# Performance work log

Measured on AMD Instinct MI355X. Metric: run time of the kernel, lower is better.

The kernel has to match this reference:

```python
import math
import jax, jax.numpy as jnp
import numpy as np

N_HEAD = 12
LN_EPS = 1e-5

def _gelu(x):
    # NewGELU: tanh approximation
    c = math.sqrt(2.0 / math.pi)
    return 0.5 * x * (1.0 + jnp.tanh(c * (x + 0.044715 * x ** 3)))

def _ln(x, w, b):
    m = x.mean(-1, keepdims=True)
    v = x.var(-1, keepdims=True)
    return (x - m) / jnp.sqrt(v + LN_EPS) * w + b

def setup_inputs() -> dict:
    key = jax.random.key(0)
    ks = jax.random.split(key, 8)
    L, C, V, BS = 12, 768, 30522, 1024
    B, T = 4, 1024
    std = 0.02
    inp = {
        'idx': jax.random.randint(ks[0], (B, T), 0, V),
        'wte': jax.random.normal(ks[1], (V, C), jnp.float32) * std,
        'wpe': jax.random.normal(ks[2], (BS, C), jnp.float32) * std,
        'ln1_w': jnp.ones((L, C), jnp.float32),
        'ln1_b': jnp.zeros((L, C), jnp.float32),
        'attn_w': jax.random.normal(ks[3], (L, 3 * C, C), jnp.float32) * std,
        'attn_b': jnp.zeros((L, 3 * C), jnp.float32),
        'proj_w': jax.random.normal(ks[4], (L, C, C), jnp.float32) * (std / math.sqrt(2 * L)),
        'proj_b': jnp.zeros((L, C), jnp.float32),
        'ln2_w': jnp.ones((L, C), jnp.float32),
        'ln2_b': jnp.zeros((L, C), jnp.float32),
        'fc_w': jax.random.normal(ks[5], (L, 4 * C, C), jnp.float32) * std,
        'fc_b': jnp.zeros((L, 4 * C), jnp.float32),
        'mproj_w': jax.random.normal(ks[6], (L, C, 4 * C), jnp.float32) * (std / math.sqrt(2 * L)),
        'mproj_b': jnp.zeros((L, C), jnp.float32),
        'lnf_w': jnp.ones((C,), jnp.float32),
        'lnf_b': jnp.zeros((C,), jnp.float32),
        'lm_head_w': jax.random.normal(ks[7], (V, C), jnp.float32) * std,
    }
    return inp

def reference(idx, wte, wpe, ln1_w, ln1_b, attn_w, attn_b, proj_w, proj_b,
              ln2_w, ln2_b, fc_w, fc_b, mproj_w, mproj_b, lnf_w, lnf_b, lm_head_w):
    B, T = idx.shape
    C = wte.shape[1]
    H = N_HEAD
    D = C // H
    scale = 1.0 / math.sqrt(D)
    x = wte[idx] + wpe[:T][None]  # [B,T,C], drop is identity (p=0)

    def block(x, p):
        l1w, l1b, aw, ab, pw, pb, l2w, l2b, fw, fb, mw, mb = p
        h = _ln(x, l1w, l1b)
        qkv = jnp.einsum('btc,ec->bte', h, aw) + ab  # [B,T,3C]
        q, k, v = jnp.split(qkv, 3, axis=-1)
        q = q.reshape(B, T, H, D)
        k = k.reshape(B, T, H, D)
        v = v.reshape(B, T, H, D)
        att = jnp.einsum('bthd,bshd->bhts', q, k) * scale  # [B,H,T,T]
        att = jax.nn.softmax(att, axis=-1)  # mask=None: full attention
        y = jnp.einsum('bhts,bshd->bthd', att, v).reshape(B, T, C)
        x = x + jnp.einsum('btc,oc->bto', y, pw) + pb
        h = _gelu(jnp.einsum('btc,fc->btf', _ln(x, l2w, l2b), fw) + fb)
        x = x + jnp.einsum('btf,cf->btc', h, mw) + mb
        return x, None

    x, _ = jax.lax.scan(block, x, (ln1_w, ln1_b, attn_w, attn_b, proj_w, proj_b,
                                   ln2_w, ln2_b, fc_w, fc_b, mproj_w, mproj_b))
    x = _ln(x, lnf_w, lnf_b)
    logits = jnp.einsum('btc,vc->btv', x, lm_head_w)  # [B,T,V]
    return logits
```

## Files before the change

kernel.cpp:

```cpp
#include <hip/hip_runtime.h>
#include <hip/hip_bf16.h>
#include <math.h>

typedef __attribute__((ext_vector_type(8))) short short8;
typedef __attribute__((ext_vector_type(4))) float f32x4;

typedef unsigned short u16;

__device__ __forceinline__ u16 f2bf(float f) {
    union { float f; unsigned int u; } v; v.f = f;
    unsigned int u = v.u;
    unsigned int r = (u + 0x7fffu + ((u >> 16) & 1u)) >> 16;
    return (u16)r;
}
__device__ __forceinline__ float bf2f(u16 u) {
    union { unsigned int u; float f; } v; v.u = ((unsigned int)u) << 16;
    return v.f;
}

__device__ __forceinline__ void gload16(const void* g, void* l) {
    __builtin_amdgcn_global_load_lds(
        (const __attribute__((address_space(1))) void*)g,
        (__attribute__((address_space(3))) void*)l, 16, 0, 0);
}

__global__ __launch_bounds__(256) void castw_kernel(const float* __restrict__ src,
                                                    u16* __restrict__ dst,
                                                    long n, long npad) {
    long i = ((long)blockIdx.x * 256 + threadIdx.x) * 4;
    const long stride = (long)gridDim.x * 1024;
    for (; i < npad; i += stride) {
        ushort4 o;
        if (i < n) {
            float4 v = *reinterpret_cast<const float4*>(src + i);
            o.x = f2bf(v.x); o.y = f2bf(v.y); o.z = f2bf(v.z); o.w = f2bf(v.w);
        } else {
            o = make_ushort4(0, 0, 0, 0);
        }
        *reinterpret_cast<ushort4*>(dst + i) = o;
    }
}

__global__ __launch_bounds__(256) void embed_kernel(const int* __restrict__ idx,
                                                    const float* __restrict__ wte,
                                                    const float* __restrict__ wpe,
                                                    float* __restrict__ x) {
    const int row = blockIdx.x;
    const int tid = threadIdx.x;
    const int t = row & 1023;
    const int tok = idx[row];
    const float* we = wte + (size_t)tok * 768;
    const float* pe = wpe + (size_t)t * 768;
    float* xr = x + (size_t)row * 768;
    xr[tid]       = we[tid]       + pe[tid];
    xr[tid + 256] = we[tid + 256] + pe[tid + 256];
    xr[tid + 512] = we[tid + 512] + pe[tid + 512];
}

__global__ __launch_bounds__(256) void ln_kernel(const float* __restrict__ x,
                                                 const float* __restrict__ w,
                                                 const float* __restrict__ b,
                                                 u16* __restrict__ out) {
    const int row = blockIdx.x;
    const int tid = threadIdx.x;
    const float* xr = x + (size_t)row * 768;
    float v0 = xr[tid], v1 = xr[tid + 256], v2 = xr[tid + 512];
    float s = v0 + v1 + v2;
    float q = v0 * v0 + v1 * v1 + v2 * v2;
    #pragma unroll
    for (int off = 32; off >= 1; off >>= 1) {
        s += __shfl_xor(s, off);
        q += __shfl_xor(q, off);
    }
    __shared__ float rs[4], rq[4];
    const int wid = tid >> 6, lane = tid & 63;
    if (lane == 0) { rs[wid] = s; rq[wid] = q; }
    __syncthreads();
    s = rs[0] + rs[1] + rs[2] + rs[3];
    q = rq[0] + rq[1] + rq[2] + rq[3];
    const float mean = s * (1.f / 768.f);
    const float var = q * (1.f / 768.f) - mean * mean;
    const float rstd = rsqrtf(var + 1e-5f);
    u16* orow = out + (size_t)row * 768;
    orow[tid]       = f2bf((v0 - mean) * rstd * w[tid]       + b[tid]);
    orow[tid + 256] = f2bf((v1 - mean) * rstd * w[tid + 256] + b[tid + 256]);
    orow[tid + 512] = f2bf((v2 - mean) * rstd * w[tid + 512] + b[tid + 512]);
}

template<int EPI>
__global__ __launch_bounds__(512) void gemm_big(
        const u16* __restrict__ A, int lda,
        const u16* __restrict__ B, int ldb,
        const float* __restrict__ bias,
        void* __restrict__ Cout, int ldc,
        int N, int K, int nmt) {
    __shared__ __align__(16) u16 lds[2][384 * 32];
    const int tid = threadIdx.x;
    const int lane = tid & 63, wid = tid >> 6;
    const int nwg = gridDim.x;
    const int o = blockIdx.x;
    const int wg = (o & 7) * (nwg >> 3) + (o >> 3);
    const int m0 = (wg % nmt) * 256, n0 = (wg / nmt) * 128;

    const int wm = (wid >> 1) * 64, wn = (wid & 1) * 64;
    const int l16 = lane & 15;
    const int qid = lane >> 4;
    const int xq8 = ((qid ^ (l16 & 3)) * 8);

    const int ar = tid >> 2, aq = (tid & 3) ^ (ar & 3);
    const size_t a_src0 = (size_t)(m0 + ar) * lda + aq * 8;
    const size_t a_src1 = (size_t)(m0 + ar + 128) * lda + aq * 8;
    const int br = tid >> 2, bq = (tid & 3) ^ (br & 3);
    const size_t b_src = (size_t)(n0 + br) * ldb + bq * 8;

    f32x4 acc[4][4];
    #pragma unroll
    for (int i = 0; i < 4; i++)
        #pragma unroll
        for (int j = 0; j < 4; j++)
            acc[i][j] = (f32x4){0.f, 0.f, 0.f, 0.f};

    const int nk = K >> 5;
    gload16(A + a_src0, lds[0] + tid * 8);
    gload16(A + a_src1, lds[0] + tid * 8 + 4096);
    gload16(B + b_src,  lds[0] + tid * 8 + 8192);

    for (int t = 0; t < nk; ++t) {
        if (t + 1 < nk) {
            u16* buf = lds[(t + 1) & 1];
            const int k0 = (t + 1) << 5;
            gload16(A + a_src0 + k0, buf + tid * 8);
            gload16(A + a_src1 + k0, buf + tid * 8 + 4096);
            gload16(B + b_src + k0,  buf + tid * 8 + 8192);
            asm volatile("s_waitcnt vmcnt(3)" ::: "memory");
        } else {
            asm volatile("s_waitcnt vmcnt(0)" ::: "memory");
        }
        __builtin_amdgcn_s_barrier();
        asm volatile("" ::: "memory");
        const u16* As = lds[t & 1];
        const u16* Bs = lds[t & 1] + 8192;
        short8 af[4], bf[4];
        #pragma unroll
        for (int i = 0; i < 4; i++) {
            af[i] = *reinterpret_cast<const short8*>(&As[(wm + i * 16 + l16) * 32 + xq8]);
            bf[i] = *reinterpret_cast<const short8*>(&Bs[(wn + i * 16 + l16) * 32 + xq8]);
        }
        #pragma unroll
        for (int mi = 0; mi < 4; mi++)
            #pragma unroll
            for (int ni = 0; ni < 4; ni++)
                acc[mi][ni] = __builtin_amdgcn_mfma_f32_16x16x32_bf16(af[mi], bf[ni], acc[mi][ni], 0, 0, 0);
        asm volatile("" ::: "memory");
        __builtin_amdgcn_s_barrier();
    }

    if (EPI == 3) {
        float* ct = reinterpret_cast<float*>(&lds[0][0]) + wid * 1088;
        const int rw = (lane >> 4) * 4;
        const int rr = lane >> 2;
        const int rc = (lane & 3) * 16;
        #pragma unroll
        for (int mi = 0; mi < 4; mi++) {
            asm volatile("" ::: "memory");
            #pragma unroll
            for (int ni = 0; ni < 4; ni++)
                #pragma unroll
                for (int j = 0; j < 4; j++)
                    ct[(rw + j) * 68 + ni * 16 + l16] = acc[mi][ni][j];
            asm volatile("" ::: "memory");
            const int m = m0 + wm + mi * 16 + rr;
            const int nb = n0 + wn + rc;
            float* crow = (float*)Cout + (size_t)m * ldc + nb;
            #pragma unroll
            for (int q = 0; q < 4; q++) {
                const f32x4 v = *reinterpret_cast<const f32x4*>(&ct[rr * 68 + rc + q * 4]);
                if (nb + q * 4 + 3 < N) {
                    *reinterpret_cast<f32x4*>(crow + q * 4) = v;
                } else {
                    #pragma unroll
                    for (int e = 0; e < 4; e++)
                        if (nb + q * 4 + e < N) crow[q * 4 + e] = v[e];
                }
            }
            asm volatile("" ::: "memory");
            __builtin_amdgcn_s_barrier();
        }
    } else {
        const int cb = n0 + wn + l16;
        const int rb = m0 + wm + (lane >> 4) * 4;
        #pragma unroll
        for (int ni = 0; ni < 4; ni++) {
            const int n = cb + ni * 16;
            const float bv = bias[n];
            #pragma unroll
            for (int mi = 0; mi < 4; mi++) {
                #pragma unroll
                for (int j = 0; j < 4; j++) {
                    const int m = rb + mi * 16 + j;
                    float v = acc[mi][ni][j] + bv;
                    if (EPI == 0) {
                        ((u16*)Cout)[(size_t)m * ldc + n] = f2bf(v);
                    } else {
                        const float t = tanhf(0.7978845608028654f * (v + 0.044715f * v * v * v));
                        ((u16*)Cout)[(size_t)m * ldc + n] = f2bf(0.5f * v * (1.f + t));
                    }
                }
            }
        }
    }
}

template<int EPI>
__global__ __launch_bounds__(256) void gemm_bb(
        const u16* __restrict__ A, int lda,
        const u16* __restrict__ B, int ldb,
        const float* __restrict__ bias,
        void* __restrict__ Cout, int ldc,
        int N, int K, int nmt,
        float* __restrict__ resid) {
    __shared__ __align__(16) u16 lds[2][2][128 * 32];
    const int tid = threadIdx.x;
    const int lane = tid & 63, wid = tid >> 6;
    const int nwg = gridDim.x;
    const int o = blockIdx.x;
    const int wg = (o & 7) * (nwg >> 3) + (o >> 3);
    const int m0 = (wg % nmt) * 128, n0 = (wg / nmt) * 128;

    const int wm = (wid >> 1) * 64, wn = (wid & 1) * 64;
    const int l16 = lane & 15;
    const int qid = lane >> 4;
    const int xq8 = ((qid ^ (l16 & 3)) * 8);

    const int r0 = tid >> 2, q0 = (tid & 3) ^ (r0 & 3);
    const size_t a_src0 = (size_t)(m0 + r0) * lda + q0 * 8;
    const size_t a_src1 = (size_t)(m0 + r0 + 64) * lda + q0 * 8;
    const size_t b_src0 = (size_t)(n0 + r0) * ldb + q0 * 8;
    const size_t b_src1 = (size_t)(n0 + r0 + 64) * ldb + q0 * 8;

    f32x4 acc[4][4];
    #pragma unroll
    for (int i = 0; i < 4; i++)
        #pragma unroll
        for (int j = 0; j < 4; j++)
            acc[i][j] = (f32x4){0.f, 0.f, 0.f, 0.f};

    const int nk = K >> 5;
    gload16(A + a_src0, lds[0][0] + tid * 8);
    gload16(A + a_src1, lds[0][0] + tid * 8 + 2048);
    gload16(B + b_src0, lds[0][1] + tid * 8);
    gload16(B + b_src1, lds[0][1] + tid * 8 + 2048);

    for (int t = 0; t < nk; ++t) {
        if (t + 1 < nk) {
            u16* Ap = lds[(t + 1) & 1][0];
            u16* Bp = lds[(t + 1) & 1][1];
            const int k0 = (t + 1) << 5;
            gload16(A + a_src0 + k0, Ap + tid * 8);
            gload16(A + a_src1 + k0, Ap + tid * 8 + 2048);
            gload16(B + b_src0 + k0, Bp + tid * 8);
            gload16(B + b_src1 + k0, Bp + tid * 8 + 2048);
            asm volatile("s_waitcnt vmcnt(4)" ::: "memory");
        } else {
            asm volatile("s_waitcnt vmcnt(0)" ::: "memory");
        }
        __builtin_amdgcn_s_barrier();
        asm volatile("" ::: "memory");
        const u16* As = lds[t & 1][0];
        const u16* Bs = lds[t & 1][1];
        short8 af[4], bf[4];
        #pragma unroll
        for (int i = 0; i < 4; i++) {
            af[i] = *reinterpret_cast<const short8*>(&As[(wm + i * 16 + l16) * 32 + xq8]);
            bf[i] = *reinterpret_cast<const short8*>(&Bs[(wn + i * 16 + l16) * 32 + xq8]);
        }
        #pragma unroll
        for (int mi = 0; mi < 4; mi++)
            #pragma unroll
            for (int ni = 0; ni < 4; ni++)
                acc[mi][ni] = __builtin_amdgcn_mfma_f32_16x16x32_bf16(af[mi], bf[ni], acc[mi][ni], 0, 0, 0);
        asm volatile("" ::: "memory");
        __builtin_amdgcn_s_barrier();
    }

    const int cb = n0 + wn + l16;
    const int rb = m0 + wm + (lane >> 4) * 4;
    #pragma unroll
    for (int ni = 0; ni < 4; ni++) {
        const int n = cb + ni * 16;
        const float bv = bias[n];
        #pragma unroll
        for (int mi = 0; mi < 4; mi++) {
            #pragma unroll
            for (int j = 0; j < 4; j++) {
                const int m = rb + mi * 16 + j;
                float v = acc[mi][ni][j] + bv;
                if (EPI == 1) {
                    resid[(size_t)m * ldc + n] += v;
                } else if (EPI == 0) {
                    ((u16*)Cout)[(size_t)m * ldc + n] = f2bf(v);
                } else {
                    const float t = tanhf(0.7978845608028654f * (v + 0.044715f * v * v * v));
                    ((u16*)Cout)[(size_t)m * ldc + n] = f2bf(0.5f * v * (1.f + t));
                }
            }
        }
    }
}

template<int EPI>
__global__ __launch_bounds__(256, 2) void gemm_bt(
        const u16* __restrict__ A, int lda,
        const float* __restrict__ B, int ldb,
        const float* __restrict__ bias,
        void* __restrict__ Cout, int ldc,
        int M, int N, int K,
        float* __restrict__ resid) {
    __shared__ __align__(16) u16 As[128][40];
    __shared__ __align__(16) u16 Bs[128][40];
    const int tid = threadIdx.x;
    const int lane = tid & 63, wid = tid >> 6;
    const int m0 = blockIdx.y * 128, n0 = blockIdx.x * 128;
    const int wm = (wid >> 1) * 64, wn = (wid & 1) * 64;
    const int l16 = lane & 15, lk = (lane >> 4) * 8;

    f32x4 acc[4][4];
    #pragma unroll
    for (int i = 0; i < 4; i++)
        #pragma unroll
        for (int j = 0; j < 4; j++)
            acc[i][j] = (f32x4){0.f, 0.f, 0.f, 0.f};

    for (int k0 = 0; k0 < K; k0 += 32) {
        #pragma unroll
        for (int p = 0; p < 2; p++) {
            const int e = p * 256 + tid;
            const int r = e >> 2, c = e & 3;
            uint4 v = *reinterpret_cast<const uint4*>(A + (size_t)(m0 + r) * lda + k0 + c * 8);
            *reinterpret_cast<uint4*>(&As[r][c * 8]) = v;
        }
        #pragma unroll
        for (int p = 0; p < 4; p++) {
            const int e = p * 256 + tid;
            const int r = e >> 3, c = e & 7;
            float4 v = make_float4(0.f, 0.f, 0.f, 0.f);
            if (n0 + r < N)
                v = *reinterpret_cast<const float4*>(B + (size_t)(n0 + r) * ldb + k0 + c * 4);
            ushort4 hv;
            hv.x = f2bf(v.x); hv.y = f2bf(v.y); hv.z = f2bf(v.z); hv.w = f2bf(v.w);
            *reinterpret_cast<ushort4*>(&Bs[r][c * 4]) = hv;
        }
        __syncthreads();
        short8 af[4], bfr[4];
        #pragma unroll
        for (int i = 0; i < 4; i++) {
            af[i]  = *reinterpret_cast<const short8*>(&As[wm + i * 16 + l16][lk]);
            bfr[i] = *reinterpret_cast<const short8*>(&Bs[wn + i * 16 + l16][lk]);
        }
        #pragma unroll
        for (int mi = 0; mi < 4; mi++)
            #pragma unroll
            for (int ni = 0; ni < 4; ni++)
                acc[mi][ni] = __builtin_amdgcn_mfma_f32_16x16x32_bf16(af[mi], bfr[ni], acc[mi][ni], 0, 0, 0);
        __syncthreads();
    }

    const int cb = n0 + wn + l16;
    const int rb = m0 + wm + (lane >> 4) * 4;
    #pragma unroll
    for (int ni = 0; ni < 4; ni++) {
        const int n = cb + ni * 16;
        if (n >= N) continue;
        float bv = 0.f;
        if (EPI != 3) bv = bias[n];
        #pragma unroll
        for (int mi = 0; mi < 4; mi++) {
            #pragma unroll
            for (int j = 0; j < 4; j++) {
                const int m = rb + mi * 16 + j;
                float v = acc[mi][ni][j] + bv;
                if (EPI == 0) {
                    ((u16*)Cout)[(size_t)m * ldc + n] = f2bf(v);
                } else if (EPI == 1) {
                    resid[(size_t)m * ldc + n] += v;
                } else if (EPI == 2) {
                    const float t = tanhf(0.7978845608028654f * (v + 0.044715f * v * v * v));
                    ((u16*)Cout)[(size_t)m * ldc + n] = f2bf(0.5f * v * (1.f + t));
                } else {
                    ((float*)Cout)[(size_t)m * ldc + n] = v;
                }
            }
        }
    }
}

__global__ __launch_bounds__(256, 2) void attn_mfma_kernel(const u16* __restrict__ qkv,
                                                           u16* __restrict__ y) {
    __shared__ __align__(16) u16 Qs[64][72];
    __shared__ __align__(16) u16 Ks[64][72];
    __shared__ __align__(16) u16 Vt[64][72];
    __shared__ __align__(16) u16 Ps[4][16][72];

    const int tid = threadIdx.x;
    const int lane = tid & 63, wid = tid >> 6;
    const int l16 = lane & 15, lk = (lane >> 4) * 8;
    const int qt = blockIdx.x, h = blockIdx.y, b = blockIdx.z;

    const size_t base = (size_t)b * 1024 * 2304;
    const u16* qp = qkv + base + (size_t)(qt * 64) * 2304 + h * 64;
    const u16* kp = qkv + base + 768  + h * 64;
    const u16* vp = qkv + base + 1536 + h * 64;

    #pragma unroll
    for (int p = 0; p < 2; p++) {
        const int e = p * 256 + tid;
        const int rr = e >> 3, c8 = e & 7;
        *reinterpret_cast<uint4*>(&Qs[rr][c8 * 8]) =
            *reinterpret_cast<const uint4*>(qp + (size_t)rr * 2304 + c8 * 8);
    }
    __syncthreads();

    short8 qf[2];
    #pragma unroll
    for (int kk = 0; kk < 2; kk++)
        qf[kk] = *reinterpret_cast<const short8*>(&Qs[wid * 16 + l16][kk * 32 + lk]);

    f32x4 o_acc[4];
    #pragma unroll
    for (int i = 0; i < 4; i++) o_acc[i] = (f32x4){0.f, 0.f, 0.f, 0.f};
    float l_part[4] = {0.f, 0.f, 0.f, 0.f};

    for (int s0 = 0; s0 < 1024; s0 += 64) {
        __syncthreads();
        #pragma unroll
        for (int p = 0; p < 2; p++) {
            const int e = p * 256 + tid;
            const int rr = e >> 3, c8 = e & 7;
            *reinterpret_cast<uint4*>(&Ks[rr][c8 * 8]) =
                *reinterpret_cast<const uint4*>(kp + (size_t)(s0 + rr) * 2304 + c8 * 8);
        }
        #pragma unroll
        for (int p = 0; p < 2; p++) {
            const int e = p * 256 + tid;
            const int s2 = e >> 4;
            const int dq = e & 15;
            const int s = s2 * 2;
            ushort4 v0 = *reinterpret_cast<const ushort4*>(vp + (size_t)(s0 + s) * 2304 + dq * 4);
            ushort4 v1 = *reinterpret_cast<const ushort4*>(vp + (size_t)(s0 + s + 1) * 2304 + dq * 4);
            *reinterpret_cast<ushort2*>(&Vt[dq * 4 + 0][s]) = make_ushort2(v0.x, v1.x);
            *reinterpret_cast<ushort2*>(&Vt[dq * 4 + 1][s]) = make_ushort2(v0.y, v1.y);
            *reinterpret_cast<ushort2*>(&Vt[dq * 4 + 2][s]) = make_ushort2(v0.z, v1.z);
            *reinterpret_cast<ushort2*>(&Vt[dq * 4 + 3][s]) = make_ushort2(v0.w, v1.w);
        }
        __syncthreads();

        f32x4 sa[4];
        #pragma unroll
        for (int i = 0; i < 4; i++) sa[i] = (f32x4){0.f, 0.f, 0.f, 0.f};
        #pragma unroll
        for (int nj = 0; nj < 4; nj++) {
            #pragma unroll
            for (int kk = 0; kk < 2; kk++) {
                short8 kf = *reinterpret_cast<const short8*>(&Ks[nj * 16 + l16][kk * 32 + lk]);
                sa[nj] = __builtin_amdgcn_mfma_f32_16x16x32_bf16(qf[kk], kf, sa[nj], 0, 0, 0);
            }
        }

        #pragma unroll
        for (int nj = 0; nj < 4; nj++) {
            #pragma unroll
            for (int r = 0; r < 4; r++) {
                const float pv = __expf(sa[nj][r] * 0.125f);
                l_part[r] += pv;
                Ps[wid][(lane >> 4) * 4 + r][nj * 16 + l16] = f2bf(pv);
            }
        }

        short8 pa[2];
        #pragma unroll
        for (int kk = 0; kk < 2; kk++)
            pa[kk] = *reinterpret_cast<const short8*>(&Ps[wid][l16][kk * 32 + lk]);
        #pragma unroll
        for (int nd = 0; nd < 4; nd++) {
            #pragma unroll
            for (int kk = 0; kk < 2; kk++) {
                short8 vf = *reinterpret_cast<const short8*>(&Vt[nd * 16 + l16][kk * 32 + lk]);
                o_acc[nd] = __builtin_amdgcn_mfma_f32_16x16x32_bf16(pa[kk], vf, o_acc[nd], 0, 0, 0);
            }
        }
    }

    float inv[4];
    #pragma unroll
    for (int r = 0; r < 4; r++) {
        float s = l_part[r];
        #pragma unroll
        for (int off = 8; off >= 1; off >>= 1) s += __shfl_xor(s, off);
        inv[r] = 1.f / s;
    }
    const int rowb = b * 1024 + qt * 64 + wid * 16 + (lane >> 4) * 4;
    #pragma unroll
    for (int nd = 0; nd < 4; nd++) {
        const int col = h * 64 + nd * 16 + l16;
        #pragma unroll
        for (int r = 0; r < 4; r++) {
            y[(size_t)(rowb + r) * 768 + col] = f2bf(o_acc[nd][r] * inv[r]);
        }
    }
}

extern "C" void kernel_launch(void* const* d_in, const int* in_sizes, int n_in,
                              void* d_out, int out_size, void* d_ws, size_t ws_size,
                              hipStream_t stream) {
    (void)in_sizes; (void)n_in; (void)out_size;
    const int*   idx    = (const int*)d_in[0];
    const float* wte    = (const float*)d_in[1];
    const float* wpe    = (const float*)d_in[2];
    const float* ln1w   = (const float*)d_in[3];
    const float* ln1b   = (const float*)d_in[4];
    const float* attnw  = (const float*)d_in[5];
    const float* attnb  = (const float*)d_in[6];
    const float* projw  = (const float*)d_in[7];
    const float* projb  = (const float*)d_in[8];
    const float* ln2w   = (const float*)d_in[9];
    const float* ln2b   = (const float*)d_in[10];
    const float* fcw    = (const float*)d_in[11];
    const float* fcb    = (const float*)d_in[12];
    const float* mprojw = (const float*)d_in[13];
    const float* mprojb = (const float*)d_in[14];
    const float* lnfw   = (const float*)d_in[15];
    const float* lnfb   = (const float*)d_in[16];
    const float* lmw    = (const float*)d_in[17];
    float* out = (float*)d_out;

    char* p = (char*)d_ws;
    size_t used = 0;
    auto take = [&](size_t bytes) { char* q = p + used; used += (bytes + 255) & ~(size_t)255; return q; };
    float* x      = (float*)take((size_t)4096 * 768 * 4);
    u16*   a_bf   = (u16*)take((size_t)4096 * 768 * 2);
    u16*   qkv_bf = (u16*)take((size_t)4096 * 2304 * 2);
    u16*   hid_bf = (u16*)take((size_t)4096 * 3072 * 2);
    u16*   w_lm   = (u16*)take((size_t)30592 * 768 * 2);
    const bool castLm = used <= ws_size;
    u16*   w_attn = (u16*)take((size_t)12 * 2304 * 768 * 2);
    u16*   w_proj = (u16*)take((size_t)12 * 768 * 768 * 2);
    u16*   w_fc   = (u16*)take((size_t)12 * 3072 * 768 * 2);
    u16*   w_mprj = (u16*)take((size_t)12 * 768 * 3072 * 2);
    const bool castAll = used <= ws_size;

    embed_kernel<<<4096, 256, 0, stream>>>(idx, wte, wpe, x);

    if (castLm)
        castw_kernel<<<2048, 256, 0, stream>>>(lmw, w_lm, (long)30522 * 768, (long)30592 * 768);
    if (castAll) {
        castw_kernel<<<2048, 256, 0, stream>>>(attnw,  w_attn, (long)12 * 2304 * 768, (long)12 * 2304 * 768);
        castw_kernel<<<2048, 256, 0, stream>>>(projw,  w_proj, (long)12 * 768 * 768,  (long)12 * 768 * 768);
        castw_kernel<<<2048, 256, 0, stream>>>(fcw,    w_fc,   (long)12 * 3072 * 768, (long)12 * 3072 * 768);
        castw_kernel<<<2048, 256, 0, stream>>>(mprojw, w_mprj, (long)12 * 768 * 3072, (long)12 * 768 * 3072);
    }

    for (int l = 0; l < 12; l++) {
        ln_kernel<<<4096, 256, 0, stream>>>(x, ln1w + l * 768, ln1b + l * 768, a_bf);
        if (castAll) {
            gemm_big<0><<<16 * 18, 512, 0, stream>>>(
                a_bf, 768, w_attn + (size_t)l * 2304 * 768, 768, attnb + l * 2304,
                (void*)qkv_bf, 2304, 2304, 768, 16);
        } else {
            gemm_bt<0><<<dim3(18, 32), 256, 0, stream>>>(
                a_bf, 768, attnw + (size_t)l * 2304 * 768, 768, attnb + l * 2304,
                (void*)qkv_bf, 2304, 4096, 2304, 768, nullptr);
        }
        attn_mfma_kernel<<<dim3(16, 12, 4), 256, 0, stream>>>(qkv_bf, a_bf);
        if (castAll) {
            gemm_bb<1><<<32 * 6, 256, 0, stream>>>(
                a_bf, 768, w_proj + (size_t)l * 768 * 768, 768, projb + l * 768,
                nullptr, 768, 768, 768, 32, x);
        } else {
            gemm_bt<1><<<dim3(6, 32), 256, 0, stream>>>(
                a_bf, 768, projw + (size_t)l * 768 * 768, 768, projb + l * 768,
                nullptr, 768, 4096, 768, 768, x);
        }
        ln_kernel<<<4096, 256, 0, stream>>>(x, ln2w + l * 768, ln2b + l * 768, a_bf);
        if (castAll) {
            gemm_big<2><<<16 * 24, 512, 0, stream>>>(
                a_bf, 768, w_fc + (size_t)l * 3072 * 768, 768, fcb + l * 3072,
                (void*)hid_bf, 3072, 3072, 768, 16);
            gemm_bb<1><<<32 * 6, 256, 0, stream>>>(
                hid_bf, 3072, w_mprj + (size_t)l * 768 * 3072, 3072, mprojb + l * 768,
                nullptr, 768, 768, 3072, 32, x);
        } else {
            gemm_bt<2><<<dim3(24, 32), 256, 0, stream>>>(
                a_bf, 768, fcw + (size_t)l * 3072 * 768, 768, fcb + l * 3072,
                (void*)hid_bf, 3072, 4096, 3072, 768, nullptr);
            gemm_bt<1><<<dim3(6, 32), 256, 0, stream>>>(
                hid_bf, 3072, mprojw + (size_t)l * 768 * 3072, 3072, mprojb + l * 768,
                nullptr, 768, 4096, 768, 3072, x);
        }
    }

    ln_kernel<<<4096, 256, 0, stream>>>(x, lnfw, lnfb, a_bf);
    if (castLm) {
        gemm_big<3><<<16 * 239, 512, 0, stream>>>(
            a_bf, 768, w_lm, 768, nullptr, (void*)out, 30522, 30522, 768, 16);
    } else {
        gemm_bt<3><<<dim3(239, 32), 256, 0, stream>>>(
            a_bf, 768, lmw, 768, nullptr, (void*)out, 30522, 4096, 30522, 768, nullptr);
    }
}
```

Baseline: 3.031 ms.

## Split-K residual GEMMs, pipeline attention K/V loads, warp-per-row LN, reorder LM-head tiles

Replaces the proj and mlp-proj GEMMs with split-K kernels that atomically add partial sums into the fp32 residual, doubling or quadrupling the workgroup count. Adds register-staged double buffering of K/V tiles in the attention kernel so global loads overlap the MFMA work. Rewrites layernorm to one wavefront per row with float4 loads and no shared-memory reduction. Adds an ORDER template so the LM-head GEMM walks N-tiles fastest. Atomics make the residual sum order nondeterministic and add contention on x.

```diff
diff --git a/kernel.cpp b/kernel.cpp
--- a/kernel.cpp
+++ b/kernel.cpp
@@ -61,33 +61,41 @@
                                                  const float* __restrict__ w,
                                                  const float* __restrict__ b,
                                                  u16* __restrict__ out) {
-    const int row = blockIdx.x;
-    const int tid = threadIdx.x;
+    const int wid = threadIdx.x >> 6, lane = threadIdx.x & 63;
+    const int row = blockIdx.x * 4 + wid;
     const float* xr = x + (size_t)row * 768;
-    float v0 = xr[tid], v1 = xr[tid + 256], v2 = xr[tid + 512];
-    float s = v0 + v1 + v2;
-    float q = v0 * v0 + v1 * v1 + v2 * v2;
+    const float4 v0 = *reinterpret_cast<const float4*>(xr + lane * 4);
+    const float4 v1 = *reinterpret_cast<const float4*>(xr + 256 + lane * 4);
+    const float4 v2 = *reinterpret_cast<const float4*>(xr + 512 + lane * 4);
+    float s = v0.x + v0.y + v0.z + v0.w + v1.x + v1.y + v1.z + v1.w
+            + v2.x + v2.y + v2.z + v2.w;
+    float q = v0.x * v0.x + v0.y * v0.y + v0.z * v0.z + v0.w * v0.w
+            + v1.x * v1.x + v1.y * v1.y + v1.z * v1.z + v1.w * v1.w
+            + v2.x * v2.x + v2.y * v2.y + v2.z * v2.z + v2.w * v2.w;
     #pragma unroll
     for (int off = 32; off >= 1; off >>= 1) {
         s += __shfl_xor(s, off);
         q += __shfl_xor(q, off);
     }
-    __shared__ float rs[4], rq[4];
-    const int wid = tid >> 6, lane = tid & 63;
-    if (lane == 0) { rs[wid] = s; rq[wid] = q; }
-    __syncthreads();
-    s = rs[0] + rs[1] + rs[2] + rs[3];
-    q = rq[0] + rq[1] + rq[2] + rq[3];
     const float mean = s * (1.f / 768.f);
     const float var = q * (1.f / 768.f) - mean * mean;
     const float rstd = rsqrtf(var + 1e-5f);
     u16* orow = out + (size_t)row * 768;
-    orow[tid]       = f2bf((v0 - mean) * rstd * w[tid]       + b[tid]);
-    orow[tid + 256] = f2bf((v1 - mean) * rstd * w[tid + 256] + b[tid + 256]);
-    orow[tid + 512] = f2bf((v2 - mean) * rstd * w[tid + 512] + b[tid + 512]);
-}
-
-template<int EPI>
+    #pragma unroll
+    for (int seg = 0; seg < 3; seg++) {
+        const float4 v = seg == 0 ? v0 : (seg == 1 ? v1 : v2);
+        const float4 wv = *reinterpret_cast<const float4*>(w + seg * 256 + lane * 4);
+        const float4 bv = *reinterpret_cast<const float4*>(b + seg * 256 + lane * 4);
+        ushort4 ov;
+        ov.x = f2bf((v.x - mean) * rstd * wv.x + bv.x);
+        ov.y = f2bf((v.y - mean) * rstd * wv.y + bv.y);
+        ov.z = f2bf((v.z - mean) * rstd * wv.z + bv.z);
+        ov.w = f2bf((v.w - mean) * rstd * wv.w + bv.w);
+        *reinterpret_cast<ushort4*>(orow + seg * 256 + lane * 4) = ov;
+    }
+}
+
+template<int EPI, int ORDER>
 __global__ __launch_bounds__(512) void gemm_big(
         const u16* __restrict__ A, int lda,
         const u16* __restrict__ B, int ldb,
@@ -100,7 +108,9 @@
     const int nwg = gridDim.x;
     const int o = blockIdx.x;
     const int wg = (o & 7) * (nwg >> 3) + (o >> 3);
-    const int m0 = (wg % nmt) * 256, n0 = (wg / nmt) * 128;
+    int m0, n0;
+    if (ORDER == 0) { m0 = (wg % nmt) * 256; n0 = (wg / nmt) * 128; }
+    else            { n0 = (wg % nmt) * 128; m0 = (wg / nmt) * 256; }
 
     const int wm = (wid >> 1) * 64, wn = (wid & 1) * 64;
     const int l16 = lane & 15;
@@ -110,8 +120,7 @@
     const int ar = tid >> 2, aq = (tid & 3) ^ (ar & 3);
     const size_t a_src0 = (size_t)(m0 + ar) * lda + aq * 8;
     const size_t a_src1 = (size_t)(m0 + ar + 128) * lda + aq * 8;
-    const int br = tid >> 2, bq = (tid & 3) ^ (br & 3);
-    const size_t b_src = (size_t)(n0 + br) * ldb + bq * 8;
+    const size_t b_src = (size_t)(n0 + ar) * ldb + aq * 8;
 
     f32x4 acc[4][4];
     #pragma unroll
@@ -211,13 +220,11 @@
     }
 }
 
-template<int EPI>
-__global__ __launch_bounds__(256) void gemm_bb(
+__global__ __launch_bounds__(256) void gemm_splitk(
         const u16* __restrict__ A, int lda,
         const u16* __restrict__ B, int ldb,
         const float* __restrict__ bias,
-        void* __restrict__ Cout, int ldc,
-        int N, int K, int nmt,
+        int ldc, int Kp, int nmt, int ntiles,
         float* __restrict__ resid) {
     __shared__ __align__(16) u16 lds[2][2][128 * 32];
     const int tid = threadIdx.x;
@@ -225,7 +232,10 @@
     const int nwg = gridDim.x;
     const int o = blockIdx.x;
     const int wg = (o & 7) * (nwg >> 3) + (o >> 3);
-    const int m0 = (wg % nmt) * 128, n0 = (wg / nmt) * 128;
+    const int tile = wg % ntiles;
+    const int ks = wg / ntiles;
+    const int m0 = (tile % nmt) * 128, n0 = (tile / nmt) * 128;
+    const int koff = ks * Kp;
 
     const int wm = (wid >> 1) * 64, wn = (wid & 1) * 64;
     const int l16 = lane & 15;
@@ -233,10 +243,10 @@
     const int xq8 = ((qid ^ (l16 & 3)) * 8);
 
     const int r0 = tid >> 2, q0 = (tid & 3) ^ (r0 & 3);
-    const size_t a_src0 = (size_t)(m0 + r0) * lda + q0 * 8;
-    const size_t a_src1 = (size_t)(m0 + r0 + 64) * lda + q0 * 8;
-    const size_t b_src0 = (size_t)(n0 + r0) * ldb + q0 * 8;
-    const size_t b_src1 = (size_t)(n0 + r0 + 64) * ldb + q0 * 8;
+    const size_t a_src0 = (size_t)(m0 + r0) * lda + koff + q0 * 8;
+    const size_t a_src1 = (size_t)(m0 + r0 + 64) * lda + koff + q0 * 8;
+    const size_t b_src0 = (size_t)(n0 + r0) * ldb + koff + q0 * 8;
+    const size_t b_src1 = (size_t)(n0 + r0 + 64) * ldb + koff + q0 * 8;
 
     f32x4 acc[4][4];
     #pragma unroll
@@ -245,7 +255,7 @@
         for (int j = 0; j < 4; j++)
             acc[i][j] = (f32x4){0.f, 0.f, 0.f, 0.f};
 
-    const int nk = K >> 5;
+    const int nk = Kp >> 5;
     gload16(A + a_src0, lds[0][0] + tid * 8);
     gload16(A + a_src1, lds[0][0] + tid * 8 + 2048);
     gload16(B + b_src0, lds[0][1] + tid * 8);
@@ -288,21 +298,13 @@
     #pragma unroll
     for (int ni = 0; ni < 4; ni++) {
         const int n = cb + ni * 16;
-        const float bv = bias[n];
+        const float bv = (ks == 0) ? bias[n] : 0.f;
         #pragma unroll
         for (int mi = 0; mi < 4; mi++) {
             #pragma unroll
             for (int j = 0; j < 4; j++) {
                 const int m = rb + mi * 16 + j;
-                float v = acc[mi][ni][j] + bv;
-                if (EPI == 1) {
-                    resid[(size_t)m * ldc + n] += v;
-                } else if (EPI == 0) {
-                    ((u16*)Cout)[(size_t)m * ldc + n] = f2bf(v);
-                } else {
-                    const float t = tanhf(0.7978845608028654f * (v + 0.044715f * v * v * v));
-                    ((u16*)Cout)[(size_t)m * ldc + n] = f2bf(0.5f * v * (1.f + t));
-                }
+                atomicAdd(&resid[(size_t)m * ldc + n], acc[mi][ni][j] + bv);
             }
         }
     }
@@ -397,8 +399,8 @@
 __global__ __launch_bounds__(256, 2) void attn_mfma_kernel(const u16* __restrict__ qkv,
                                                            u16* __restrict__ y) {
     __shared__ __align__(16) u16 Qs[64][72];
-    __shared__ __align__(16) u16 Ks[64][72];
-    __shared__ __align__(16) u16 Vt[64][72];
+    __shared__ __align__(16) u16 Ks[2][64][72];
+    __shared__ __align__(16) u16 Vt[2][64][72];
     __shared__ __align__(16) u16 Ps[4][16][72];
 
     const int tid = threadIdx.x;
@@ -410,6 +412,11 @@
     const u16* qp = qkv + base + (size_t)(qt * 64) * 2304 + h * 64;
     const u16* kp = qkv + base + 768  + h * 64;
     const u16* vp = qkv + base + 1536 + h * 64;
+
+    const int krr0 = tid >> 3, kc8_0 = tid & 7;
+    const int krr1 = (tid + 256) >> 3, kc8_1 = tid & 7;
+    const int vs0 = (tid >> 4) * 2, vdq0 = tid & 15;
+    const int vs1 = ((tid + 256) >> 4) * 2, vdq1 = tid & 15;
 
     #pragma unroll
     for (int p = 0; p < 2; p++) {
@@ -418,6 +425,13 @@
         *reinterpret_cast<uint4*>(&Qs[rr][c8 * 8]) =
             *reinterpret_cast<const uint4*>(qp + (size_t)rr * 2304 + c8 * 8);
     }
+    uint4 kreg0, kreg1; ushort4 vr0a, vr0b, vr1a, vr1b;
+    kreg0 = *reinterpret_cast<const uint4*>(kp + (size_t)krr0 * 2304 + kc8_0 * 8);
+    kreg1 = *reinterpret_cast<const uint4*>(kp + (size_t)krr1 * 2304 + kc8_1 * 8);
+    vr0a = *reinterpret_cast<const ushort4*>(vp + (size_t)vs0 * 2304 + vdq0 * 4);
+    vr0b = *reinterpret_cast<const ushort4*>(vp + (size_t)(vs0 + 1) * 2304 + vdq0 * 4);
+    vr1a = *reinterpret_cast<const ushort4*>(vp + (size_t)vs1 * 2304 + vdq1 * 4);
+    vr1b = *reinterpret_cast<const ushort4*>(vp + (size_t)(vs1 + 1) * 2304 + vdq1 * 4);
     __syncthreads();
 
     short8 qf[2];
@@ -425,34 +439,34 @@
     for (int kk = 0; kk < 2; kk++)
         qf[kk] = *reinterpret_cast<const short8*>(&Qs[wid * 16 + l16][kk * 32 + lk]);
 
+    *reinterpret_cast<uint4*>(&Ks[0][krr0][kc8_0 * 8]) = kreg0;
+    *reinterpret_cast<uint4*>(&Ks[0][krr1][kc8_1 * 8]) = kreg1;
+    *reinterpret_cast<ushort2*>(&Vt[0][vdq0 * 4 + 0][vs0]) = make_ushort2(vr0a.x, vr0b.x);
+    *reinterpret_cast<ushort2*>(&Vt[0][vdq0 * 4 + 1][vs0]) = make_ushort2(vr0a.y, vr0b.y);
+    *reinterpret_cast<ushort2*>(&Vt[0][vdq0 * 4 + 2][vs0]) = make_ushort2(vr0a.z, vr0b.z);
+    *reinterpret_cast<ushort2*>(&Vt[0][vdq0 * 4 + 3][vs0]) = make_ushort2(vr0a.w, vr0b.w);
+    *reinterpret_cast<ushort2*>(&Vt[0][vdq1 * 4 + 0][vs1]) = make_ushort2(vr1a.x, vr1b.x);
+    *reinterpret_cast<ushort2*>(&Vt[0][vdq1 * 4 + 1][vs1]) = make_ushort2(vr1a.y, vr1b.y);
+    *reinterpret_cast<ushort2*>(&Vt[0][vdq1 * 4 + 2][vs1]) = make_ushort2(vr1a.z, vr1b.z);
+    *reinterpret_cast<ushort2*>(&Vt[0][vdq1 * 4 + 3][vs1]) = make_ushort2(vr1a.w, vr1b.w);
+    __syncthreads();
+
     f32x4 o_acc[4];
     #pragma unroll
     for (int i = 0; i < 4; i++) o_acc[i] = (f32x4){0.f, 0.f, 0.f, 0.f};
     float l_part[4] = {0.f, 0.f, 0.f, 0.f};
 
-    for (int s0 = 0; s0 < 1024; s0 += 64) {
-        __syncthreads();
-        #pragma unroll
-        for (int p = 0; p < 2; p++) {
-            const int e = p * 256 + tid;
-            const int rr = e >> 3, c8 = e & 7;
-            *reinterpret_cast<uint4*>(&Ks[rr][c8 * 8]) =
-                *reinterpret_cast<const uint4*>(kp + (size_t)(s0 + rr) * 2304 + c8 * 8);
-        }
-        #pragma unroll
-        for (int p = 0; p < 2; p++) {
-            const int e = p * 256 + tid;
-            const int s2 = e >> 4;
-            const int dq = e & 15;
-            const int s = s2 * 2;
-            ushort4 v0 = *reinterpret_cast<const ushort4*>(vp + (size_t)(s0 + s) * 2304 + dq * 4);
-            ushort4 v1 = *reinterpret_cast<const ushort4*>(vp + (size_t)(s0 + s + 1) * 2304 + dq * 4);
-            *reinterpret_cast<ushort2*>(&Vt[dq * 4 + 0][s]) = make_ushort2(v0.x, v1.x);
-            *reinterpret_cast<ushort2*>(&Vt[dq * 4 + 1][s]) = make_ushort2(v0.y, v1.y);
-            *reinterpret_cast<ushort2*>(&Vt[dq * 4 + 2][s]) = make_ushort2(v0.z, v1.z);
-            *reinterpret_cast<ushort2*>(&Vt[dq * 4 + 3][s]) = make_ushort2(v0.w, v1.w);
-        }
-        __syncthreads();
+    for (int t = 0; t < 16; ++t) {
+        const int cur = t & 1, nxt = cur ^ 1;
+        if (t + 1 < 16) {
+            const int s0 = (t + 1) * 64;
+            kreg0 = *reinterpret_cast<const uint4*>(kp + (size_t)(s0 + krr0) * 2304 + kc8_0 * 8);
+            kreg1 = *reinterpret_cast<const uint4*>(kp + (size_t)(s0 + krr1) * 2304 + kc8_1 * 8);
+            vr0a = *reinterpret_cast<const ushort4*>(vp + (size_t)(s0 + vs0) * 2304 + vdq0 * 4);
+            vr0b = *reinterpret_cast<const ushort4*>(vp + (size_t)(s0 + vs0 + 1) * 2304 + vdq0 * 4);
+            vr1a = *reinterpret_cast<const ushort4*>(vp + (size_t)(s0 + vs1) * 2304 + vdq1 * 4);
+            vr1b = *reinterpret_cast<const ushort4*>(vp + (size_t)(s0 + vs1 + 1) * 2304 + vdq1 * 4);
+        }
 
         f32x4 sa[4];
         #pragma unroll
@@ -461,11 +475,10 @@
         for (int nj = 0; nj < 4; nj++) {
             #pragma unroll
             for (int kk = 0; kk < 2; kk++) {
-                short8 kf = *reinterpret_cast<const short8*>(&Ks[nj * 16 + l16][kk * 32 + lk]);
+                short8 kf = *reinterpret_cast<const short8*>(&Ks[cur][nj * 16 + l16][kk * 32 + lk]);
                 sa[nj] = __builtin_amdgcn_mfma_f32_16x16x32_bf16(qf[kk], kf, sa[nj], 0, 0, 0);
             }
         }
-
         #pragma unroll
         for (int nj = 0; nj < 4; nj++) {
             #pragma unroll
@@ -475,7 +488,6 @@
                 Ps[wid][(lane >> 4) * 4 + r][nj * 16 + l16] = f2bf(pv);
             }
         }
-
         short8 pa[2];
         #pragma unroll
         for (int kk = 0; kk < 2; kk++)
@@ -484,10 +496,24 @@
         for (int nd = 0; nd < 4; nd++) {
             #pragma unroll
             for (int kk = 0; kk < 2; kk++) {
-                short8 vf = *reinterpret_cast<const short8*>(&Vt[nd * 16 + l16][kk * 32 + lk]);
+                short8 vf = *reinterpret_cast<const short8*>(&Vt[cur][nd * 16 + l16][kk * 32 + lk]);
                 o_acc[nd] = __builtin_amdgcn_mfma_f32_16x16x32_bf16(pa[kk], vf, o_acc[nd], 0, 0, 0);
             }
         }
+
+        if (t + 1 < 16) {
+            *reinterpret_cast<uint4*>(&Ks[nxt][krr0][kc8_0 * 8]) = kreg0;
+            *reinterpret_cast<uint4*>(&Ks[nxt][krr1][kc8_1 * 8]) = kreg1;
+            *reinterpret_cast<ushort2*>(&Vt[nxt][vdq0 * 4 + 0][vs0]) = make_ushort2(vr0a.x, vr0b.x);
+            *reinterpret_cast<ushort2*>(&Vt[nxt][vdq0 * 4 + 1][vs0]) = make_ushort2(vr0a.y, vr0b.y);
+            *reinterpret_cast<ushort2*>(&Vt[nxt][vdq0 * 4 + 2][vs0]) = make_ushort2(vr0a.z, vr0b.z);
+            *reinterpret_cast<ushort2*>(&Vt[nxt][vdq0 * 4 + 3][vs0]) = make_ushort2(vr0a.w, vr0b.w);
+            *reinterpret_cast<ushort2*>(&Vt[nxt][vdq1 * 4 + 0][vs1]) = make_ushort2(vr1a.x, vr1b.x);
+            *reinterpret_cast<ushort2*>(&Vt[nxt][vdq1 * 4 + 1][vs1]) = make_ushort2(vr1a.y, vr1b.y);
+            *reinterpret_cast<ushort2*>(&Vt[nxt][vdq1 * 4 + 2][vs1]) = make_ushort2(vr1a.z, vr1b.z);
+            *reinterpret_cast<ushort2*>(&Vt[nxt][vdq1 * 4 + 3][vs1]) = make_ushort2(vr1a.w, vr1b.w);
+        }
+        __syncthreads();
     }
 
     float inv[4];
@@ -560,9 +586,9 @@
     }
 
     for (int l = 0; l < 12; l++) {
-        ln_kernel<<<4096, 256, 0, stream>>>(x, ln1w + l * 768, ln1b + l * 768, a_bf);
+        ln_kernel<<<1024, 256, 0, stream>>>(x, ln1w + l * 768, ln1b + l * 768, a_bf);
         if (castAll) {
-            gemm_big<0><<<16 * 18, 512, 0, stream>>>(
+            gemm_big<0, 0><<<16 * 18, 512, 0, stream>>>(
                 a_bf, 768, w_attn + (size_t)l * 2304 * 768, 768, attnb + l * 2304,
                 (void*)qkv_bf, 2304, 2304, 768, 16);
         } else {
@@ -572,22 +598,22 @@
         }
         attn_mfma_kernel<<<dim3(16, 12, 4), 256, 0, stream>>>(qkv_bf, a_bf);
         if (castAll) {
-            gemm_bb<1><<<32 * 6, 256, 0, stream>>>(
+            gemm_splitk<<<192 * 2, 256, 0, stream>>>(
                 a_bf, 768, w_proj + (size_t)l * 768 * 768, 768, projb + l * 768,
-                nullptr, 768, 768, 768, 32, x);
+                768, 384, 32, 192, x);
         } else {
             gemm_bt<1><<<dim3(6, 32), 256, 0, stream>>>(
                 a_bf, 768, projw + (size_t)l * 768 * 768, 768, projb + l * 768,
                 nullptr, 768, 4096, 768, 768, x);
         }
-        ln_kernel<<<4096, 256, 0, stream>>>(x, ln2w + l * 768, ln2b + l * 768, a_bf);
+        ln_kernel<<<1024, 256, 0, stream>>>(x, ln2w + l * 768, ln2b + l * 768, a_bf);
         if (castAll) {
-            gemm_big<2><<<16 * 24, 512, 0, stream>>>(
+            gemm_big<2, 0><<<16 * 24, 512, 0, stream>>>(
                 a_bf, 768, w_fc + (size_t)l * 3072 * 768, 768, fcb + l * 3072,
                 (void*)hid_bf, 3072, 3072, 768, 16);
-            gemm_bb<1><<<32 * 6, 256, 0, stream>>>(
+            gemm_splitk<<<192 * 4, 256, 0, stream>>>(
                 hid_bf, 3072, w_mprj + (size_t)l * 768 * 3072, 3072, mprojb + l * 768,
-                nullptr, 768, 768, 3072, 32, x);
+                768, 768, 32, 192, x);
         } else {
             gemm_bt<2><<<dim3(24, 32), 256, 0, stream>>>(
                 a_bf, 768, fcw + (size_t)l * 3072 * 768, 768, fcb + l * 3072,
@@ -598,10 +624,10 @@
         }
     }
 
-    ln_kernel<<<4096, 256, 0, stream>>>(x, lnfw, lnfb, a_bf);
+    ln_kernel<<<1024, 256, 0, stream>>>(x, lnfw, lnfb, a_bf);
     if (castLm) {
-        gemm_big<3><<<16 * 239, 512, 0, stream>>>(
-            a_bf, 768, w_lm, 768, nullptr, (void*)out, 30522, 30522, 768, 16);
+        gemm_big<3, 1><<<16 * 239, 512, 0, stream>>>(
+            a_bf, 768, w_lm, 768, nullptr, (void*)out, 30522, 30522, 768, 239);
     } else {
         gemm_bt<3><<<dim3(239, 32), 256, 0, stream>>>(
             a_bf, 768, lmw, 768, nullptr, (void*)out, 30522, 4096, 30522, 768, nullptr);
```

Result: no change. 3.039 ms (+0.3%).
